# Kernel optimization log

Measured on AMD Instinct MI355X. Metric: run time of the kernel, lower is better.

## Reference

```python
import jax, jax.numpy as jnp
import numpy as np
import math

EMBED_DIM = 1024
NUM_HEADS = 16
HEAD_DIM = EMBED_DIM // NUM_HEADS
BATCH = 2
SEQ = 2048


def setup_inputs() -> dict:
    key = jax.random.key(0)
    ks = jax.random.split(key, 9)
    s = 1.0 / math.sqrt(EMBED_DIM)
    return {
        "x": jax.random.normal(ks[0], (BATCH, SEQ, EMBED_DIM), jnp.float32),
        "Wq": jax.random.normal(ks[1], (EMBED_DIM, EMBED_DIM), jnp.float32) * s,
        "bq": jnp.zeros((EMBED_DIM,), jnp.float32),
        "Wk": jax.random.normal(ks[2], (EMBED_DIM, EMBED_DIM), jnp.float32) * s,
        "bk": jnp.zeros((EMBED_DIM,), jnp.float32),
        "Wv": jax.random.normal(ks[3], (EMBED_DIM, EMBED_DIM), jnp.float32) * s,
        "bv": jnp.zeros((EMBED_DIM,), jnp.float32),
        "Wo": jax.random.normal(ks[4], (EMBED_DIM, EMBED_DIM), jnp.float32) * s,
        "bo": jnp.zeros((EMBED_DIM,), jnp.float32),
    }


def _rope_tables(seq_len, dim, dtype):
    inv_freq = 1.0 / (10000.0 ** (jnp.arange(0, dim, 2, dtype=jnp.float32) / dim))
    t = jnp.arange(seq_len, dtype=jnp.float32)
    freqs = jnp.einsum("i,j->ij", t, inv_freq)          # [S, D/2]
    emb = jnp.concatenate([freqs, freqs], axis=-1)       # [S, D]
    return jnp.cos(emb).astype(dtype), jnp.sin(emb).astype(dtype)


def _rotate_half(x):
    x1, x2 = jnp.split(x, 2, axis=-1)
    return jnp.concatenate([-x2, x1], axis=-1)


def _apply_rope(x, cos, sin):
    # x: [B, S, H, D]; cos/sin: [S, D] -> broadcast over batch & heads
    cos = cos[None, :, None, :]
    sin = sin[None, :, None, :]
    return x * cos + _rotate_half(x) * sin


def reference(x, Wq, bq, Wk, bk, Wv, bv, Wo, bo):
    B, S, E = x.shape
    H, D = NUM_HEADS, HEAD_DIM
    q = (x @ Wq + bq).reshape(B, S, H, D)
    k = (x @ Wk + bk).reshape(B, S, H, D)
    v = (x @ Wv + bv).reshape(B, S, H, D)
    cos, sin = _rope_tables(S, D, x.dtype)
    q = _apply_rope(q, cos, sin)
    k = _apply_rope(k, cos, sin)
    scale = 1.0 / math.sqrt(D)
    # scores: [B, H, S, S]
    scores = jnp.einsum("bqhd,bkhd->bhqk", q, k) * scale
    attn = jax.nn.softmax(scores, axis=-1)
    ctx = jnp.einsum("bhqk,bkhd->bqhd", attn, v).reshape(B, S, E)
    return ctx @ Wo + bo
```

## Files before the change

### kernel.cpp

```cpp
#include <hip/hip_runtime.h>
#include <math.h>

#define B_ 2
#define S_ 2048
#define E_ 1024
#define H_ 16
#define D_ 64
#define M_ (B_*S_)

typedef _Float16 f16x8  __attribute__((ext_vector_type(8)));
typedef _Float16 f16x4v __attribute__((ext_vector_type(4)));
typedef __fp16   h16x2  __attribute__((ext_vector_type(2)));
typedef float    f32x4  __attribute__((ext_vector_type(4)));

__device__ __forceinline__ ushort f2h(float f) {
    _Float16 h = (_Float16)f;
    return __builtin_bit_cast(ushort, h);
}

__device__ __forceinline__ void gload_lds16(const ushort* g, ushort* l) {
    __builtin_amdgcn_global_load_lds(
        (const __attribute__((address_space(1))) unsigned int*)g,
        (__attribute__((address_space(3))) unsigned int*)l, 16, 0, 0);
}

__global__ void prep_kernel(const float* __restrict__ x,
                            const float* __restrict__ W0, const float* __restrict__ W1,
                            const float* __restrict__ W2, const float* __restrict__ W3,
                            ushort* __restrict__ xf, ushort* __restrict__ WT,
                            float* __restrict__ ct, float* __restrict__ st)
{
    const int bid = blockIdx.x;
    const int tid = threadIdx.x;
    __shared__ float tile[32][33];

    if (bid < 4096) {
        const int z = bid >> 10, rem = bid & 1023;
        const int k0 = (rem >> 5) * 32, nb = (rem & 31) * 32;
        const float* W = (z == 0) ? W0 : (z == 1) ? W1 : (z == 2) ? W2 : W3;
        const size_t zoff = (size_t)z * E_ * E_;
        const int tx = tid & 31, ty = tid >> 5;
        #pragma unroll
        for (int i = 0; i < 4; i++) {
            int r = i * 8 + ty;
            tile[r][tx] = W[(size_t)(k0 + r) * E_ + nb + tx];
        }
        __syncthreads();
        #pragma unroll
        for (int i = 0; i < 4; i++) {
            int r = i * 8 + ty;
            WT[zoff + (size_t)(nb + r) * E_ + k0 + tx] = f2h(tile[tx][r]);
        }
    } else if (bid < 8192) {
        const int i = (bid - 4096) * 1024 + tid * 4;
        float4 v = *(const float4*)&x[i];
        *(ushort4*)&xf[i] = make_ushort4(f2h(v.x), f2h(v.y), f2h(v.z), f2h(v.w));
    } else {
        const int i = (bid - 8192) * 256 + tid;
        const int j = i & 31, pos = i >> 5;
        float invf = (float)pow(10000.0, -(double)j / 32.0);
        float ang  = (float)pos * invf;
        ct[i] = (float)cos((double)ang);
        st[i] = (float)sin((double)ang);
    }
}

#define GBM 128
#define GBN 128
#define GBK 32

__global__ __launch_bounds__(256, 3)
void gemm_f16(const ushort* __restrict__ A, const ushort* __restrict__ WTp,
              const float* __restrict__ b0, const float* __restrict__ b1,
              const float* __restrict__ b2,
              const float* __restrict__ ct, const float* __restrict__ st,
              ushort* __restrict__ outQ, ushort* __restrict__ outK,
              ushort* __restrict__ outV, float* __restrict__ outF,
              int force_mode)
{
    __shared__ __align__(16) ushort lA[GBM * GBK];
    __shared__ __align__(16) ushort lB[GBN * GBK];

    const int tid  = threadIdx.x;
    const int wv   = tid >> 6, lane = tid & 63;
    const int c    = lane & 15, qd = lane >> 4;
    const int rh   = wv >> 1, chn = wv & 1;

    const int mode = (force_mode >= 0) ? force_mode : (int)blockIdx.z;
    const size_t zoff = (force_mode >= 0) ? 0 : (size_t)blockIdx.z * (E_ * E_);
    const ushort* Bt = WTp + zoff;

    const int m0 = blockIdx.y * GBM, n0 = blockIdx.x * GBN;

    const ushort* gsrc = (wv < 2) ? A : Bt;
    ushort* ldst = (wv < 2) ? lA : lB;
    const int rowbase = ((wv < 2) ? m0 : n0) + (wv & 1) * 64;
    const int lofs = (wv & 1) * 64 * GBK;
    const int srow = lane >> 2;
    const int soct = (lane & 3) * 8;

    f32x4 acc[4][4] = {};

    for (int k0i = 0; k0i < E_; k0i += GBK) {
        #pragma unroll
        for (int cc = 0; cc < 4; cc++) {
            const ushort* g = gsrc + (size_t)(rowbase + cc * 16 + srow) * E_ + k0i + soct;
            gload_lds16(g, ldst + lofs + cc * 512);
        }
        __syncthreads();

        f16x8 af[4], bf[4];
        #pragma unroll
        for (int mt = 0; mt < 4; mt++)
            af[mt] = *(const f16x8*)&lA[(rh * 64 + mt * 16 + c) * GBK + qd * 8];
        #pragma unroll
        for (int nt = 0; nt < 4; nt++)
            bf[nt] = *(const f16x8*)&lB[(chn * 64 + nt * 16 + c) * GBK + qd * 8];
        #pragma unroll
        for (int mt = 0; mt < 4; mt++)
            #pragma unroll
            for (int nt = 0; nt < 4; nt++)
                acc[mt][nt] = __builtin_amdgcn_mfma_f32_16x16x32_f16(af[mt], bf[nt], acc[mt][nt], 0, 0, 0);
        __syncthreads();
    }

    const float* bias = (mode == 0) ? b0 : (mode == 1) ? b1 : (mode == 2) ? b2 : b0;
    const int colbase = n0 + chn * 64;

    if (mode == 3) {
        #pragma unroll
        for (int mt = 0; mt < 4; mt++)
            #pragma unroll
            for (int r = 0; r < 4; r++) {
                const int row = m0 + rh * 64 + mt * 16 + qd * 4 + r;
                #pragma unroll
                for (int nt = 0; nt < 4; nt++) {
                    const int col = colbase + nt * 16 + c;
                    outF[(size_t)row * E_ + col] = acc[mt][nt][r] + bias[col];
                }
            }
    } else if (mode == 2) {
        const int hd = colbase >> 6;
        #pragma unroll
        for (int mt = 0; mt < 4; mt++)
            #pragma unroll
            for (int r = 0; r < 4; r++) {
                const int row = m0 + rh * 64 + mt * 16 + qd * 4 + r;
                const int bb = row >> 11, sl = row & (S_ - 1);
                const int tt = sl >> 7, key = sl & 127;
                const int c4 = key >> 2, inner = key & 3;
                const size_t base = (size_t)(bb * H_ + hd) * (S_ * D_) + tt * 8192;
                #pragma unroll
                for (int nt = 0; nt < 4; nt++) {
                    const int d = nt * 16 + c;
                    outV[base + d * 128 + ((c4 ^ (d & 7)) * 4) + inner]
                        = f2h(acc[mt][nt][r] + bias[colbase + d]);
                }
            }
    } else {
        ushort* O = (mode == 0) ? outQ : outK;
        const float sc = (mode == 0) ? 0.125f : 1.0f;
        #pragma unroll
        for (int mt = 0; mt < 4; mt++)
            #pragma unroll
            for (int r = 0; r < 4; r++) {
                const int row = m0 + rh * 64 + mt * 16 + qd * 4 + r;
                const int pos = row & (S_ - 1);
                const int sw = row & 7;
                #pragma unroll
                for (int p = 0; p < 2; p++) {
                    const int j32 = p * 16 + c;
                    const float cth = ct[pos * 32 + j32], sth = st[pos * 32 + j32];
                    const float v1 = acc[mt][p][r]     + bias[colbase + p * 16 + c];
                    const float v2 = acc[mt][p + 2][r] + bias[colbase + (p + 2) * 16 + c];
                    const float o1 = (v1 * cth - v2 * sth) * sc;
                    const float o2 = (v2 * cth + v1 * sth) * sc;
                    const int cd1 = p * 16 + c, cd2 = cd1 + 32;
                    O[(size_t)row * E_ + colbase + (((cd1 >> 3) ^ sw) * 8) + (cd1 & 7)] = f2h(o1);
                    O[(size_t)row * E_ + colbase + (((cd2 >> 3) ^ sw) * 8) + (cd2 & 7)] = f2h(o2);
                }
            }
    }
}

__global__ __launch_bounds__(256, 3)
void attn_mfma(const ushort* __restrict__ Qf, const ushort* __restrict__ Kf,
               const ushort* __restrict__ Vfg, ushort* __restrict__ ctxf)
{
    __shared__ __align__(16) ushort Kls[128 * 64];
    __shared__ __align__(16) ushort Vls[64 * 128];

    const int tid = threadIdx.x;
    const int wv = tid >> 6, lane = tid & 63;
    const int c = lane & 15, qd = lane >> 4;
    const int cs = c & 7;

    const int xcd = blockIdx.x & 7, ii = blockIdx.x >> 3;
    const int bh = xcd * 4 + (ii & 3);
    const int qtb = ii >> 2;
    const int b = bh >> 4, h = bh & 15;
    const int q0 = qtb * 64;

    const size_t qrow0 = (size_t)b * S_ + q0;
    const size_t krow0 = (size_t)b * S_;
    const size_t vbase = (size_t)bh * (S_ * D_);

    const int l8 = lane >> 3, l7 = lane & 7;
    const int l16 = lane >> 4, l15 = lane & 15;

    #pragma unroll
    for (int j = 0; j < 2; j++) {
        const int row = wv * 16 + j * 8 + l8;
        const ushort* g = Qf + (qrow0 + row) * E_ + h * 64 + l7 * 8;
        gload_lds16(g, Kls + wv * 1024 + j * 512);
    }
    __syncthreads();
    f16x8 qfrag[4][2];
    #pragma unroll
    for (int qt = 0; qt < 4; qt++)
        #pragma unroll
        for (int kc = 0; kc < 2; kc++)
            qfrag[qt][kc] = *(const f16x8*)&Kls[(qt * 16 + c) * 64 + (((kc * 4 + qd) ^ cs) * 8)];
    __syncthreads();

    f32x4 acc[4][4] = {};
    float lsum[4] = {0.f, 0.f, 0.f, 0.f};

    #pragma unroll 1
    for (int t = 0; t < 16; t++) {
        const int k0 = t * 128;
        if (wv < 2) {
            #pragma unroll
            for (int j = 0; j < 8; j++) {
                const int row = wv * 64 + j * 8 + l8;
                const ushort* g = Kf + (krow0 + k0 + row) * E_ + h * 64 + l7 * 8;
                gload_lds16(g, Kls + wv * 4096 + j * 512);
            }
        } else {
            #pragma unroll
            for (int j = 0; j < 8; j++) {
                const int drow = (wv - 2) * 32 + j * 4 + l16;
                const ushort* g = Vfg + vbase + t * 8192 + drow * 128 + l15 * 8;
                gload_lds16(g, Vls + (wv - 2) * 4096 + j * 512);
            }
        }
        __syncthreads();

        f16x4v bfrag[2][4];
        #pragma unroll
        for (int kt = 0; kt < 2; kt++) {
            f16x8 kfr[2];
            #pragma unroll
            for (int kc = 0; kc < 2; kc++)
                kfr[kc] = *(const f16x8*)&Kls[(wv * 32 + kt * 16 + c) * 64 + (((kc * 4 + qd) ^ cs) * 8)];
            #pragma unroll
            for (int qt = 0; qt < 4; qt++) {
                f32x4 s = {};
                s = __builtin_amdgcn_mfma_f32_16x16x32_f16(kfr[0], qfrag[qt][0], s, 0, 0, 0);
                s = __builtin_amdgcn_mfma_f32_16x16x32_f16(kfr[1], qfrag[qt][1], s, 0, 0, 0);
                const float p0 = __expf(s[0]), p1 = __expf(s[1]);
                const float p2 = __expf(s[2]), p3 = __expf(s[3]);
                lsum[qt] += (p0 + p1) + (p2 + p3);
                h16x2 lo = __builtin_amdgcn_cvt_pkrtz(p0, p1);
                h16x2 hi = __builtin_amdgcn_cvt_pkrtz(p2, p3);
                uint2 u;
                u.x = __builtin_bit_cast(unsigned int, lo);
                u.y = __builtin_bit_cast(unsigned int, hi);
                bfrag[kt][qt] = __builtin_bit_cast(f16x4v, u);
            }
        }

        #pragma unroll
        for (int dt = 0; dt < 4; dt++) {
            #pragma unroll
            for (int kt = 0; kt < 2; kt++) {
                f16x4v vfr = *(const f16x4v*)&Vls[(dt * 16 + c) * 128 + (((wv * 8 + kt * 4 + qd) ^ cs) * 4)];
                #pragma unroll
                for (int qt = 0; qt < 4; qt++)
                    acc[dt][qt] = __builtin_amdgcn_mfma_f32_16x16x16f16(vfr, bfrag[kt][qt], acc[dt][qt], 0, 0, 0);
            }
        }
        __syncthreads();
    }

    float* red = (float*)Kls;
    float* lsr = (float*)Vls;

    #pragma unroll
    for (int qt = 0; qt < 4; qt++) {
        float v = lsum[qt];
        v += __shfl_xor(v, 16);
        v += __shfl_xor(v, 32);
        lsum[qt] = v;
    }
    if (lane < 16) {
        #pragma unroll
        for (int qt = 0; qt < 4; qt++) lsr[wv * 64 + qt * 16 + lane] = lsum[qt];
    }

    f32x4 own[4];
    #pragma unroll
    for (int qt = 0; qt < 4; qt++)
        own[qt] = (wv == 0) ? acc[0][qt] : (wv == 1) ? acc[1][qt]
                : (wv == 2) ? acc[2][qt] : acc[3][qt];

    #pragma unroll
    for (int r = 1; r < 4; r++) {
        const int ds = (wv + r) & 3;
        #pragma unroll
        for (int qt = 0; qt < 4; qt++) {
            f32x4 sv = (ds == 0) ? acc[0][qt] : (ds == 1) ? acc[1][qt]
                     : (ds == 2) ? acc[2][qt] : acc[3][qt];
            *(f32x4*)&red[ds * 1024 + qt * 256 + lane * 4] = sv;
        }
        __syncthreads();
        #pragma unroll
        for (int qt = 0; qt < 4; qt++)
            own[qt] += *(const f32x4*)&red[wv * 1024 + qt * 256 + lane * 4];
        if (r < 3) __syncthreads();
    }

    float inv[4];
    #pragma unroll
    for (int qt = 0; qt < 4; qt++) {
        const int q = qt * 16 + c;
        inv[qt] = 1.0f / (lsr[q] + lsr[64 + q] + lsr[128 + q] + lsr[192 + q]);
    }

    const size_t obase = qrow0 * E_ + h * 64 + wv * 16 + qd * 4;
    #pragma unroll
    for (int qt = 0; qt < 4; qt++) {
        f32x4 v = own[qt];
        const float iq = inv[qt];
        ushort4 o = make_ushort4(f2h(v[0] * iq), f2h(v[1] * iq),
                                 f2h(v[2] * iq), f2h(v[3] * iq));
        *(ushort4*)&ctxf[obase + (size_t)(qt * 16 + c) * E_] = o;
    }
}

extern "C" void kernel_launch(void* const* d_in, const int* in_sizes, int n_in,
                              void* d_out, int out_size, void* d_ws, size_t ws_size,
                              hipStream_t stream)
{
    const float* x  = (const float*)d_in[0];
    const float* Wq = (const float*)d_in[1];
    const float* bq = (const float*)d_in[2];
    const float* Wk = (const float*)d_in[3];
    const float* bk = (const float*)d_in[4];
    const float* Wv = (const float*)d_in[5];
    const float* bv = (const float*)d_in[6];
    const float* Wo = (const float*)d_in[7];
    const float* bo = (const float*)d_in[8];
    float* out = (float*)d_out;

    ushort* Qb = (ushort*)d_ws;
    ushort* Kb = Qb + (size_t)M_ * E_;
    ushort* Vf = Kb + (size_t)M_ * E_;
    ushort* xf = Vf + (size_t)M_ * E_;
    ushort* WT = xf + (size_t)M_ * E_;
    float*  ct = (float*)(WT + (size_t)4 * E_ * E_);
    float*  st = ct + S_ * 32;
    ushort* ctxf = Qb;

    hipLaunchKernelGGL(prep_kernel, dim3(8448), dim3(256), 0, stream,
                       x, Wq, Wk, Wv, Wo, xf, WT, ct, st);

    hipLaunchKernelGGL(gemm_f16, dim3(E_ / GBN, M_ / GBM, 3), dim3(256), 0, stream,
                       xf, WT, bq, bk, bv, ct, st,
                       Qb, Kb, Vf, (float*)nullptr, -1);

    hipLaunchKernelGGL(attn_mfma, dim3(B_ * H_ * (S_ / 64)), dim3(256), 0, stream,
                       Qb, Kb, Vf, ctxf);

    hipLaunchKernelGGL(gemm_f16, dim3(E_ / GBN, M_ / GBM, 1), dim3(256), 0, stream,
                       ctxf, WT + (size_t)3 * E_ * E_, bo, bo, bo, ct, st,
                       (ushort*)nullptr, (ushort*)nullptr, (ushort*)nullptr, out, 3);
}
```

Baseline: 210.9 us.

## Double-buffer K/V tiles in attention and interleave QKV projection blocks

The attention kernel gets two LDS buffers for K and V so the next tile's global-to-LDS load is issued before the current tile is computed. This removes one barrier per iteration and hides load latency, at the cost of doubled LDS and occupancy dropped from 3 to 2 blocks per CU. The QKV GEMM launch is flattened so the Q/K/V mode comes from blockIdx.x % 3, interleaving the three projections across neighbouring blocks for better A-tile reuse in cache.

New measurement: 215.6 us. +2.2%, slower.

```diff
diff --git a/kernel.cpp b/kernel.cpp
--- a/kernel.cpp
+++ b/kernel.cpp
@@ -86,11 +86,13 @@
     const int c    = lane & 15, qd = lane >> 4;
     const int rh   = wv >> 1, chn = wv & 1;
 
-    const int mode = (force_mode >= 0) ? force_mode : (int)blockIdx.z;
-    const size_t zoff = (force_mode >= 0) ? 0 : (size_t)blockIdx.z * (E_ * E_);
+    int mode, nx;
+    size_t zoff;
+    if (force_mode >= 0) { mode = force_mode; nx = blockIdx.x; zoff = 0; }
+    else { mode = blockIdx.x % 3; nx = blockIdx.x / 3; zoff = (size_t)mode * (E_ * E_); }
     const ushort* Bt = WTp + zoff;
 
-    const int m0 = blockIdx.y * GBM, n0 = blockIdx.x * GBN;
+    const int m0 = blockIdx.y * GBM, n0 = nx * GBN;
 
     const ushort* gsrc = (wv < 2) ? A : Bt;
     ushort* ldst = (wv < 2) ? lA : lB;
@@ -183,12 +185,12 @@
     }
 }
 
-__global__ __launch_bounds__(256, 3)
+__global__ __launch_bounds__(256, 2)
 void attn_mfma(const ushort* __restrict__ Qf, const ushort* __restrict__ Kf,
                const ushort* __restrict__ Vfg, ushort* __restrict__ ctxf)
 {
-    __shared__ __align__(16) ushort Kls[128 * 64];
-    __shared__ __align__(16) ushort Vls[64 * 128];
+    __shared__ __align__(16) ushort Kls[2][128 * 64];
+    __shared__ __align__(16) ushort Vls[2][64 * 128];
 
     const int tid = threadIdx.x;
     const int wv = tid >> 6, lane = tid & 63;
@@ -212,7 +214,7 @@
     for (int j = 0; j < 2; j++) {
         const int row = wv * 16 + j * 8 + l8;
         const ushort* g = Qf + (qrow0 + row) * E_ + h * 64 + l7 * 8;
-        gload_lds16(g, Kls + wv * 1024 + j * 512);
+        gload_lds16(g, &Kls[0][wv * 1024 + j * 512]);
     }
     __syncthreads();
     f16x8 qfrag[4][2];
@@ -220,31 +222,53 @@
     for (int qt = 0; qt < 4; qt++)
         #pragma unroll
         for (int kc = 0; kc < 2; kc++)
-            qfrag[qt][kc] = *(const f16x8*)&Kls[(qt * 16 + c) * 64 + (((kc * 4 + qd) ^ cs) * 8)];
+            qfrag[qt][kc] = *(const f16x8*)&Kls[0][(qt * 16 + c) * 64 + (((kc * 4 + qd) ^ cs) * 8)];
     __syncthreads();
 
     f32x4 acc[4][4] = {};
     float lsum[4] = {0.f, 0.f, 0.f, 0.f};
 
+    if (wv < 2) {
+        #pragma unroll
+        for (int j = 0; j < 8; j++) {
+            const int row = wv * 64 + j * 8 + l8;
+            gload_lds16(Kf + (krow0 + row) * E_ + h * 64 + l7 * 8,
+                        &Kls[0][wv * 4096 + j * 512]);
+        }
+    } else {
+        #pragma unroll
+        for (int j = 0; j < 8; j++) {
+            const int drow = (wv - 2) * 32 + j * 4 + l16;
+            gload_lds16(Vfg + vbase + drow * 128 + l15 * 8,
+                        &Vls[0][(wv - 2) * 4096 + j * 512]);
+        }
+    }
+    __syncthreads();
+
     #pragma unroll 1
     for (int t = 0; t < 16; t++) {
-        const int k0 = t * 128;
-        if (wv < 2) {
-            #pragma unroll
-            for (int j = 0; j < 8; j++) {
-                const int row = wv * 64 + j * 8 + l8;
-                const ushort* g = Kf + (krow0 + k0 + row) * E_ + h * 64 + l7 * 8;
-                gload_lds16(g, Kls + wv * 4096 + j * 512);
-            }
-        } else {
-            #pragma unroll
-            for (int j = 0; j < 8; j++) {
-                const int drow = (wv - 2) * 32 + j * 4 + l16;
-                const ushort* g = Vfg + vbase + t * 8192 + drow * 128 + l15 * 8;
-                gload_lds16(g, Vls + (wv - 2) * 4096 + j * 512);
-            }
-        }
-        __syncthreads();
+        if (t < 15) {
+            const int nb = (t + 1) & 1;
+            const int k0n = (t + 1) * 128;
+            if (wv < 2) {
+                #pragma unroll
+                for (int j = 0; j < 8; j++) {
+                    const int row = wv * 64 + j * 8 + l8;
+                    gload_lds16(Kf + (krow0 + k0n + row) * E_ + h * 64 + l7 * 8,
+                                &Kls[nb][wv * 4096 + j * 512]);
+                }
+            } else {
+                #pragma unroll
+                for (int j = 0; j < 8; j++) {
+                    const int drow = (wv - 2) * 32 + j * 4 + l16;
+                    gload_lds16(Vfg + vbase + (t + 1) * 8192 + drow * 128 + l15 * 8,
+                                &Vls[nb][(wv - 2) * 4096 + j * 512]);
+                }
+            }
+        }
+
+        const ushort* kb = Kls[t & 1];
+        const ushort* vb = Vls[t & 1];
 
         f16x4v bfrag[2][4];
         #pragma unroll
@@ -252,7 +276,7 @@
             f16x8 kfr[2];
             #pragma unroll
             for (int kc = 0; kc < 2; kc++)
-                kfr[kc] = *(const f16x8*)&Kls[(wv * 32 + kt * 16 + c) * 64 + (((kc * 4 + qd) ^ cs) * 8)];
+                kfr[kc] = *(const f16x8*)&kb[(wv * 32 + kt * 16 + c) * 64 + (((kc * 4 + qd) ^ cs) * 8)];
             #pragma unroll
             for (int qt = 0; qt < 4; qt++) {
                 f32x4 s = {};
@@ -274,7 +298,7 @@
         for (int dt = 0; dt < 4; dt++) {
             #pragma unroll
             for (int kt = 0; kt < 2; kt++) {
-                f16x4v vfr = *(const f16x4v*)&Vls[(dt * 16 + c) * 128 + (((wv * 8 + kt * 4 + qd) ^ cs) * 4)];
+                f16x4v vfr = *(const f16x4v*)&vb[(dt * 16 + c) * 128 + (((wv * 8 + kt * 4 + qd) ^ cs) * 4)];
                 #pragma unroll
                 for (int qt = 0; qt < 4; qt++)
                     acc[dt][qt] = __builtin_amdgcn_mfma_f32_16x16x16f16(vfr, bfrag[kt][qt], acc[dt][qt], 0, 0, 0);
@@ -283,8 +307,8 @@
         __syncthreads();
     }
 
-    float* red = (float*)Kls;
-    float* lsr = (float*)Vls;
+    float* red = (float*)&Kls[0][0];
+    float* lsr = (float*)&Vls[0][0];
 
     #pragma unroll
     for (int qt = 0; qt < 4; qt++) {
@@ -365,14 +389,14 @@
     hipLaunchKernelGGL(prep_kernel, dim3(8448), dim3(256), 0, stream,
                        x, Wq, Wk, Wv, Wo, xf, WT, ct, st);
 
-    hipLaunchKernelGGL(gemm_f16, dim3(E_ / GBN, M_ / GBM, 3), dim3(256), 0, stream,
+    hipLaunchKernelGGL(gemm_f16, dim3(24, 32), dim3(256), 0, stream,
                        xf, WT, bq, bk, bv, ct, st,
                        Qb, Kb, Vf, (float*)nullptr, -1);
 
     hipLaunchKernelGGL(attn_mfma, dim3(B_ * H_ * (S_ / 64)), dim3(256), 0, stream,
                        Qb, Kb, Vf, ctxf);
 
-    hipLaunchKernelGGL(gemm_f16, dim3(E_ / GBN, M_ / GBM, 1), dim3(256), 0, stream,
+    hipLaunchKernelGGL(gemm_f16, dim3(E_ / GBN, M_ / GBM), dim3(256), 0, stream,
                        ctxf, WT + (size_t)3 * E_ * E_, bo, bo, bo, ct, st,
                        (ushort*)nullptr, (ushort*)nullptr, (ushort*)nullptr, out, 3);
 }
```
